# Optimization experiments

Measured on AMD Instinct MI355X. Metric: run time of the kernel, lower is better.

## Reference

```python
import jax, jax.numpy as jnp
import numpy as np

SIZE = 128      # reconstruction grid (size x size)
ANGLES = 128    # number of projection angles after interpolation
B, C, H, W = 2, 8, 128, 128  # batch, channels, detector rows (z-slices), detector cols
N_VIEWS = 8


def setup_inputs() -> dict:
    key = jax.random.key(0)
    keys = jax.random.split(key, N_VIEWS)
    return {f"f{i}": jax.random.normal(keys[i], (B, C, H, W), dtype=jnp.float32)
            for i in range(N_VIEWS)}


def _fbp(projections, size, n_angles):
    # projections: (B, C, H, V, W) -- V stacked views, W detector columns
    b, c, h, v, w = projections.shape
    # Interpolation step: resize V views -> n_angles angles (linear, half-pixel,
    # matching F.interpolate default semantics)
    sino = jax.image.resize(projections, (b, c, h, n_angles, w), method="linear")
    # Ram-Lak ramp filter along the detector-column axis
    ramp = jnp.abs(jnp.fft.fftfreq(w)).astype(jnp.float32)
    filt = jnp.real(jnp.fft.ifft(jnp.fft.fft(sino, axis=-1) * ramp, axis=-1)).astype(sino.dtype)
    # Back-projection (parallel beam, per z-slice H)
    thetas = jnp.arange(n_angles, dtype=jnp.float32) * (jnp.pi / n_angles)
    xs = jnp.arange(size, dtype=jnp.float32) - (size - 1) / 2.0
    X, Y = jnp.meshgrid(xs, xs, indexing="xy")  # (S, S)
    center = (w - 1) / 2.0

    sino_per_angle = jnp.moveaxis(filt, 3, 0)  # (A, B, C, H, W)

    def body(acc, inputs):
        theta, sino_a = inputs                       # sino_a: (B, C, H, W)
        t = X * jnp.cos(theta) + Y * jnp.sin(theta) + center  # (S, S)
        t = jnp.clip(t, 0.0, w - 1.0)
        t0 = jnp.floor(t).astype(jnp.int32)
        t1 = jnp.minimum(t0 + 1, w - 1)
        w1 = (t - t0).astype(sino_a.dtype)
        v0 = sino_a[..., t0]                         # (B, C, H, S, S) gather
        v1 = sino_a[..., t1]
        acc = acc + v0 * (1.0 - w1) + v1 * w1
        return acc, None

    acc0 = jnp.zeros((b, c, h, size, size), dtype=sino.dtype)
    vol, _ = jax.lax.scan(body, acc0, (thetas, sino_per_angle))
    return vol * (jnp.pi / (2.0 * n_angles))


def reference(f0, f1, f2, f3, f4, f5, f6, f7):
    # torch.cat([f.unsqueeze(3) for f in features], dim=3) == stack on new axis 3
    projections = jnp.stack([f0, f1, f2, f3, f4, f5, f6, f7], axis=3)  # (B,C,H,V,W)
    return _fbp(projections, SIZE, ANGLES)
```

## Files before the change

kernel.cpp:

```cpp
#include <hip/hip_runtime.h>
#include <math.h>

#define W 128
#define NANG 128
#define SZ 128
#define NV 8
#define NROWS 2048
#define K_DIM 1024
#define NPIX 16384
#define OUT_SCALE 0.012271846303085130f

typedef _Float16 f16x8 __attribute__((ext_vector_type(8)));
typedef _Float16 f16x4 __attribute__((ext_vector_type(4)));
typedef float    f32x4 __attribute__((ext_vector_type(4)));

#define PF_OFF 36864
#define WV_OFF (36864 + (size_t)NROWS * K_DIM * 2)

struct Ptrs8 { const float* p[8]; };

__device__ __forceinline__ void glds16(const void* g, void* l) {
    __builtin_amdgcn_global_load_lds(
        (const __attribute__((address_space(1))) void*)g,
        (__attribute__((address_space(3))) void*)l, 16, 0, 0);
}

#define FS_A 136
#define PREP_FG_BLOCKS 256

union PrepLds {
    struct {
        _Float16 sA[64 * FS_A];
        _Float16 sB[128 * FS_A];
        float    kl[W];
    } fg;
    struct {
        float  wrow[8 * K_DIM];
        float2 cst[NANG];
    } wv;
};

__global__ __launch_bounds__(256)
void k_prep(Ptrs8 in, _Float16* __restrict__ pf, _Float16* __restrict__ wv) {
    __shared__ PrepLds u;
    const int tid = threadIdx.x;

    if (blockIdx.x < PREP_FG_BLOCKS) {
        const int blk  = blockIdx.x;
        const int lane = tid & 63, wave = tid >> 6;
        const int fr = lane & 15, fg = lane >> 4;

        if (tid < W) {
            const int d = tid;
            const float w0 = 6.283185307179586f / (float)W * (float)d;
            float s = 0.f;
            for (int f = 1; f < 64; ++f)
                s = fmaf((float)f, __cosf(w0 * (float)f), s);
            s = 2.f * s + 64.f * ((d & 1) ? -1.f : 1.f);
            u.fg.kl[d] = s * (1.f / (float)(W * W));
        }
        {
            const int i   = tid >> 5;
            const int pos = (tid & 31) * 4;
#pragma unroll
            for (int v = 0; v < NV; ++v) {
                float4 x = *(const float4*)(in.p[v] + (size_t)(blk * 8 + i) * W + pos);
                f16x4 h = { (_Float16)x.x, (_Float16)x.y, (_Float16)x.z, (_Float16)x.w };
                *(f16x4*)&u.fg.sA[(i * 8 + v) * FS_A + pos] = h;
            }
        }
        __syncthreads();
        for (int e = tid; e < W * W; e += 256) {
            const int t = e >> 7, s = e & 127;
            u.fg.sB[t * FS_A + s] = (_Float16)u.fg.kl[(t - s) & (W - 1)];
        }
        __syncthreads();

        f32x4 acc[8] = {};
#pragma unroll
        for (int kb = 0; kb < W; kb += 32) {
            f16x8 af = *(const f16x8*)&u.fg.sA[(wave * 16 + fr) * FS_A + kb + fg * 8];
#pragma unroll
            for (int nt = 0; nt < 8; ++nt) {
                f16x8 bf = *(const f16x8*)&u.fg.sB[(nt * 16 + fr) * FS_A + kb + fg * 8];
                acc[nt] = __builtin_amdgcn_mfma_f32_16x16x32_f16(af, bf, acc[nt], 0, 0, 0);
            }
        }
#pragma unroll
        for (int nt = 0; nt < 8; ++nt) {
            int m = blk * 64 + wave * 16 + fg * 4;
            int n = nt * 16 + fr;
#pragma unroll
            for (int rr = 0; rr < 4; ++rr)
                pf[(size_t)(m + rr) * W + n] = (_Float16)acc[nt][rr];
        }
    } else {
        const int p0 = (blockIdx.x - PREP_FG_BLOCKS) * 8;
        if (tid < NANG) {
            float th = (float)tid * ((float)M_PI / (float)NANG);
            u.wv.cst[tid] = make_float2(cosf(th), sinf(th));
        }
        for (int i = tid; i < 8 * K_DIM; i += 256) u.wv.wrow[i] = 0.f;
        __syncthreads();
        const int px  = tid >> 5;
        const int sub = tid & 31;
        const int p = p0 + px;
        const float x = (float)(p & 127) - 63.5f;
        const float y = (float)(p >> 7) - 63.5f;
        float* prow = &u.wv.wrow[px * K_DIM];
        for (int a = sub; a < NANG; a += 32) {
            float2 c = u.wv.cst[a];
            float t = fmaf(x, c.x, fmaf(y, c.y, 63.5f));
            t = fminf(fmaxf(t, 0.f), 127.f);
            float tf = fminf(floorf(t), 126.f);
            int   ti = (int)tf;
            float wt = t - tf;
            float src = ((float)a + 0.5f) * 0.0625f - 0.5f;
            src = fminf(fmaxf(src, 0.f), 7.f);
            float vf = floorf(src);
            int   v0 = (int)vf;
            int   v1 = v0 + 1 < NV ? v0 + 1 : NV - 1;
            float wa = src - vf;
            float wA0 = (1.f - wa) * OUT_SCALE;
            atomicAdd(&prow[v0 * W + ti],     wA0 * (1.f - wt));
            atomicAdd(&prow[v0 * W + ti + 1], wA0 * wt);
            if (v1 != v0) {
                float wA1 = wa * OUT_SCALE;
                atomicAdd(&prow[v1 * W + ti],     wA1 * (1.f - wt));
                atomicAdd(&prow[v1 * W + ti + 1], wA1 * wt);
            }
        }
        __syncthreads();
        uint* wvu = (uint*)(wv + (size_t)p0 * K_DIM);
#pragma unroll
        for (int j = 0; j < 16; ++j) {
            int j2 = tid + 256 * j;
            float2 w2 = *(const float2*)&u.wv.wrow[j2 * 2];
            union { uint uu; struct { _Float16 lo, hi; } h; } pk;
            pk.h.lo = (_Float16)w2.x; pk.h.hi = (_Float16)w2.y;
            wvu[j2] = pk.uu;
        }
    }
}

#define NT 16

__device__ __forceinline__ void fencebar() {
    asm volatile("" ::: "memory");
    __builtin_amdgcn_s_barrier();
    asm volatile("" ::: "memory");
}

__device__ __forceinline__ void stage_half(const _Float16* __restrict__ G, int R0,
                                           int h, int kt, _Float16* L, int tid) {
#pragma unroll
    for (int r = 0; r < 2; ++r) {
        const int c   = r * 512 + tid;
        const int row = (h << 7) + (c >> 3);
        const int q   = c & 7;
        const _Float16* src = G + (size_t)(R0 + row) * K_DIM + kt * 64
                                + ((q ^ (row & 7)) << 3);
        _Float16* dst = L + (h << 13) + ((r * 512 + (tid & 448)) << 3);
        glds16(src, dst);
    }
}

__device__ __forceinline__ f16x8 frag(const _Float16* L, int row, int q) {
    return *(const f16x8*)(L + row * 64 + ((q ^ (row & 7)) << 3));
}

__global__ __launch_bounds__(512, 2)
void k_gemm(const _Float16* __restrict__ A,
            const _Float16* __restrict__ Bm,
            float* __restrict__ out) {
    __shared__ _Float16 lds[65536];
    const int tid  = threadIdx.x;
    const int lane = tid & 63, wid = tid >> 6;
    const int wm = wid >> 2, wn = wid & 3;
    const int fr = lane & 15, fg = lane >> 4;

    const int flat = blockIdx.y * 64 + blockIdx.x;
    const int x    = flat & 7;
    const int idx  = flat >> 3;
    const int m0 = (idx >> 3) * 256;
    const int n0 = (x * 8 + (idx & 7)) * 256;

    _Float16* const A0 = lds;
    _Float16* const B0 = lds + 16384;
    _Float16* const A1 = lds + 32768;
    _Float16* const B1 = lds + 49152;

    stage_half(Bm, n0, 0, 0, B0, tid);
    stage_half(A,  m0, 0, 0, A0, tid);
    stage_half(Bm, n0, 1, 0, B0, tid);
    stage_half(A,  m0, 1, 0, A0, tid);
    stage_half(Bm, n0, 0, 1, B1, tid);
    stage_half(A,  m0, 0, 1, A1, tid);
    asm volatile("s_waitcnt vmcnt(4)" ::: "memory");
    fencebar();

    f32x4 acc[8][4] = {};
    f16x8 af[4][2], bf[4][2];
    const int ar = wm * 128 + fr;
    const int br = wn * 64 + fr;

    auto tile = [&](int t, _Float16* Ab, _Float16* Bb, _Float16* An, _Float16* Bn)
        __attribute__((always_inline)) {
        if (t + 1 < NT) stage_half(Bm, n0, 1, t + 1, Bn, tid);
#pragma unroll
        for (int i = 0; i < 4; ++i) {
            af[i][0] = frag(Ab, ar + i * 16, fg);
            af[i][1] = frag(Ab, ar + i * 16, 4 + fg);
        }
#pragma unroll
        for (int j = 0; j < 2; ++j) {
            bf[j][0] = frag(Bb, br + j * 16, fg);
            bf[j][1] = frag(Bb, br + j * 16, 4 + fg);
        }
        __builtin_amdgcn_s_setprio(1);
#pragma unroll
        for (int i = 0; i < 4; ++i)
#pragma unroll
            for (int j = 0; j < 2; ++j) {
                acc[i][j] = __builtin_amdgcn_mfma_f32_16x16x32_f16(af[i][0], bf[j][0], acc[i][j], 0, 0, 0);
                acc[i][j] = __builtin_amdgcn_mfma_f32_16x16x32_f16(af[i][1], bf[j][1], acc[i][j], 0, 0, 0);
            }
        __builtin_amdgcn_s_setprio(0);
        asm volatile("s_waitcnt lgkmcnt(0)" ::: "memory");
        fencebar();
        if (t + 1 < NT) stage_half(A, m0, 1, t + 1, An, tid);
#pragma unroll
        for (int j = 2; j < 4; ++j) {
            bf[j][0] = frag(Bb, br + j * 16, fg);
            bf[j][1] = frag(Bb, br + j * 16, 4 + fg);
        }
        __builtin_amdgcn_s_setprio(1);
#pragma unroll
        for (int i = 0; i < 4; ++i)
#pragma unroll
            for (int j = 2; j < 4; ++j) {
                acc[i][j] = __builtin_amdgcn_mfma_f32_16x16x32_f16(af[i][0], bf[j][0], acc[i][j], 0, 0, 0);
                acc[i][j] = __builtin_amdgcn_mfma_f32_16x16x32_f16(af[i][1], bf[j][1], acc[i][j], 0, 0, 0);
            }
        __builtin_amdgcn_s_setprio(0);
        asm volatile("s_waitcnt lgkmcnt(0)" ::: "memory");
        fencebar();
        if (t + 2 < NT) stage_half(Bm, n0, 0, t + 2, Bb, tid);
#pragma unroll
        for (int i = 0; i < 4; ++i) {
            af[i][0] = frag(Ab, ar + 64 + i * 16, fg);
            af[i][1] = frag(Ab, ar + 64 + i * 16, 4 + fg);
        }
        __builtin_amdgcn_s_setprio(1);
#pragma unroll
        for (int i = 0; i < 4; ++i)
#pragma unroll
            for (int j = 2; j < 4; ++j) {
                acc[4 + i][j] = __builtin_amdgcn_mfma_f32_16x16x32_f16(af[i][0], bf[j][0], acc[4 + i][j], 0, 0, 0);
                acc[4 + i][j] = __builtin_amdgcn_mfma_f32_16x16x32_f16(af[i][1], bf[j][1], acc[4 + i][j], 0, 0, 0);
            }
        __builtin_amdgcn_s_setprio(0);
        asm volatile("s_waitcnt lgkmcnt(0)" ::: "memory");
        fencebar();
        if (t + 2 < NT) stage_half(A, m0, 0, t + 2, Ab, tid);
        __builtin_amdgcn_s_setprio(1);
#pragma unroll
        for (int i = 0; i < 4; ++i)
#pragma unroll
            for (int j = 0; j < 2; ++j) {
                acc[4 + i][j] = __builtin_amdgcn_mfma_f32_16x16x32_f16(af[i][0], bf[j][0], acc[4 + i][j], 0, 0, 0);
                acc[4 + i][j] = __builtin_amdgcn_mfma_f32_16x16x32_f16(af[i][1], bf[j][1], acc[4 + i][j], 0, 0, 0);
            }
        __builtin_amdgcn_s_setprio(0);
        if (t + 2 < NT)      asm volatile("s_waitcnt vmcnt(4)" ::: "memory");
        else if (t + 1 < NT) asm volatile("s_waitcnt vmcnt(0)" ::: "memory");
        fencebar();
    };

    for (int tt = 0; tt < NT; tt += 2) {
        tile(tt,     A0, B0, A1, B1);
        tile(tt + 1, A1, B1, A0, B0);
    }

#pragma unroll
    for (int i = 0; i < 8; ++i) {
#pragma unroll
        for (int j = 0; j < 4; ++j) {
            const int m = m0 + wm * 128 + i * 16 + fg * 4;
            const int n = n0 + wn * 64 + j * 16 + fr;
            float* op = out + (size_t)m * NPIX + n;
#pragma unroll
            for (int rr = 0; rr < 4; ++rr)
                op[(size_t)rr * NPIX] = acc[i][j][rr];
        }
    }
}

extern "C" void kernel_launch(void* const* d_in, const int* in_sizes, int n_in,
                              void* d_out, int out_size, void* d_ws, size_t ws_size,
                              hipStream_t stream) {
    _Float16*   pf = (_Float16*)((char*)d_ws + PF_OFF);
    _Float16*   wv = (_Float16*)((char*)d_ws + WV_OFF);

    Ptrs8 in;
    for (int i = 0; i < NV; ++i) in.p[i] = (const float*)d_in[i];

    k_prep<<<PREP_FG_BLOCKS + NPIX / 8, 256, 0, stream>>>(in, pf, wv);
    dim3 grid(NPIX / 256, NROWS / 256);
    k_gemm<<<grid, 512, 0, stream>>>(pf, wv, (float*)d_out);
}
```

Baseline: 258.0 us.

## Shrink GEMM tiles to 128x128 with BK=32 and 256-thread blocks

Replaces the 256x256 tile, 512-thread GEMM (BK=64, 128KB LDS, split-phase staging) with a 128x128 tile, 256-thread kernel using BK=32 double buffering and 32KB LDS. The aim is higher occupancy (4 blocks per CU) and more blocks to fill the machine, replacing the intricate interleaved staging schedule with a simpler full-stage-then-compute loop. In exchange, global traffic per flop doubles, and each K step waits for all outstanding loads (vmcnt(0)), which can expose memory latency.

```diff
diff --git a/kernel.cpp b/kernel.cpp
--- a/kernel.cpp
+++ b/kernel.cpp
@@ -143,7 +143,7 @@
     }
 }
 
-#define NT 16
+#define NT3 32
 
 __device__ __forceinline__ void fencebar() {
     asm volatile("" ::: "memory");
@@ -151,142 +151,89 @@
     asm volatile("" ::: "memory");
 }
 
-__device__ __forceinline__ void stage_half(const _Float16* __restrict__ G, int R0,
-                                           int h, int kt, _Float16* L, int tid) {
+__device__ __forceinline__ void stage3(const _Float16* __restrict__ G, int R0,
+                                       int kt, _Float16* L, int tid) {
 #pragma unroll
     for (int r = 0; r < 2; ++r) {
-        const int c   = r * 512 + tid;
-        const int row = (h << 7) + (c >> 3);
-        const int q   = c & 7;
-        const _Float16* src = G + (size_t)(R0 + row) * K_DIM + kt * 64
-                                + ((q ^ (row & 7)) << 3);
-        _Float16* dst = L + (h << 13) + ((r * 512 + (tid & 448)) << 3);
+        const int c   = r * 256 + tid;
+        const int row = c >> 2;
+        const int q   = c & 3;
+        const _Float16* src = G + (size_t)(R0 + row) * K_DIM + kt * 32
+                                + ((q ^ (row & 3)) << 3);
+        _Float16* dst = L + ((r * 256 + (tid & 192)) << 3);
         glds16(src, dst);
     }
 }
 
-__device__ __forceinline__ f16x8 frag(const _Float16* L, int row, int q) {
-    return *(const f16x8*)(L + row * 64 + ((q ^ (row & 7)) << 3));
-}
-
-__global__ __launch_bounds__(512, 2)
+__device__ __forceinline__ f16x8 frag3(const _Float16* L, int row, int q) {
+    return *(const f16x8*)(L + row * 32 + ((q ^ (row & 3)) << 3));
+}
+
+__global__ __launch_bounds__(256, 4)
 void k_gemm(const _Float16* __restrict__ A,
             const _Float16* __restrict__ Bm,
             float* __restrict__ out) {
-    __shared__ _Float16 lds[65536];
+    __shared__ _Float16 lds[16384];
     const int tid  = threadIdx.x;
     const int lane = tid & 63, wid = tid >> 6;
-    const int wm = wid >> 2, wn = wid & 3;
+    const int wm = wid >> 1, wn = wid & 1;
     const int fr = lane & 15, fg = lane >> 4;
 
-    const int flat = blockIdx.y * 64 + blockIdx.x;
+    const int flat = blockIdx.x;
     const int x    = flat & 7;
     const int idx  = flat >> 3;
-    const int m0 = (idx >> 3) * 256;
-    const int n0 = (x * 8 + (idx & 7)) * 256;
+    const int m0 = (idx & 15) * 128;
+    const int n0 = (x * 16 + (idx >> 4)) * 128;
 
     _Float16* const A0 = lds;
-    _Float16* const B0 = lds + 16384;
-    _Float16* const A1 = lds + 32768;
-    _Float16* const B1 = lds + 49152;
-
-    stage_half(Bm, n0, 0, 0, B0, tid);
-    stage_half(A,  m0, 0, 0, A0, tid);
-    stage_half(Bm, n0, 1, 0, B0, tid);
-    stage_half(A,  m0, 1, 0, A0, tid);
-    stage_half(Bm, n0, 0, 1, B1, tid);
-    stage_half(A,  m0, 0, 1, A1, tid);
-    asm volatile("s_waitcnt vmcnt(4)" ::: "memory");
+    _Float16* const B0 = lds + 4096;
+    _Float16* const A1 = lds + 8192;
+    _Float16* const B1 = lds + 12288;
+
+    stage3(A,  m0, 0, A0, tid);
+    stage3(Bm, n0, 0, B0, tid);
+    asm volatile("s_waitcnt vmcnt(0)" ::: "memory");
     fencebar();
 
-    f32x4 acc[8][4] = {};
-    f16x8 af[4][2], bf[4][2];
-    const int ar = wm * 128 + fr;
+    f32x4 acc[4][4] = {};
+    f16x8 af[4], bf[4];
+    const int ar = wm * 64 + fr;
     const int br = wn * 64 + fr;
 
     auto tile = [&](int t, _Float16* Ab, _Float16* Bb, _Float16* An, _Float16* Bn)
         __attribute__((always_inline)) {
-        if (t + 1 < NT) stage_half(Bm, n0, 1, t + 1, Bn, tid);
-#pragma unroll
-        for (int i = 0; i < 4; ++i) {
-            af[i][0] = frag(Ab, ar + i * 16, fg);
-            af[i][1] = frag(Ab, ar + i * 16, 4 + fg);
-        }
-#pragma unroll
-        for (int j = 0; j < 2; ++j) {
-            bf[j][0] = frag(Bb, br + j * 16, fg);
-            bf[j][1] = frag(Bb, br + j * 16, 4 + fg);
-        }
+        if (t + 1 < NT3) {
+            stage3(A,  m0, t + 1, An, tid);
+            stage3(Bm, n0, t + 1, Bn, tid);
+        }
+#pragma unroll
+        for (int i = 0; i < 4; ++i) af[i] = frag3(Ab, ar + i * 16, fg);
+#pragma unroll
+        for (int j = 0; j < 4; ++j) bf[j] = frag3(Bb, br + j * 16, fg);
         __builtin_amdgcn_s_setprio(1);
 #pragma unroll
         for (int i = 0; i < 4; ++i)
 #pragma unroll
-            for (int j = 0; j < 2; ++j) {
-                acc[i][j] = __builtin_amdgcn_mfma_f32_16x16x32_f16(af[i][0], bf[j][0], acc[i][j], 0, 0, 0);
-                acc[i][j] = __builtin_amdgcn_mfma_f32_16x16x32_f16(af[i][1], bf[j][1], acc[i][j], 0, 0, 0);
-            }
+            for (int j = 0; j < 4; ++j)
+                acc[i][j] = __builtin_amdgcn_mfma_f32_16x16x32_f16(
+                    af[i], bf[j], acc[i][j], 0, 0, 0);
         __builtin_amdgcn_s_setprio(0);
         asm volatile("s_waitcnt lgkmcnt(0)" ::: "memory");
-        fencebar();
-        if (t + 1 < NT) stage_half(A, m0, 1, t + 1, An, tid);
-#pragma unroll
-        for (int j = 2; j < 4; ++j) {
-            bf[j][0] = frag(Bb, br + j * 16, fg);
-            bf[j][1] = frag(Bb, br + j * 16, 4 + fg);
-        }
-        __builtin_amdgcn_s_setprio(1);
-#pragma unroll
-        for (int i = 0; i < 4; ++i)
-#pragma unroll
-            for (int j = 2; j < 4; ++j) {
-                acc[i][j] = __builtin_amdgcn_mfma_f32_16x16x32_f16(af[i][0], bf[j][0], acc[i][j], 0, 0, 0);
-                acc[i][j] = __builtin_amdgcn_mfma_f32_16x16x32_f16(af[i][1], bf[j][1], acc[i][j], 0, 0, 0);
-            }
-        __builtin_amdgcn_s_setprio(0);
-        asm volatile("s_waitcnt lgkmcnt(0)" ::: "memory");
-        fencebar();
-        if (t + 2 < NT) stage_half(Bm, n0, 0, t + 2, Bb, tid);
-#pragma unroll
-        for (int i = 0; i < 4; ++i) {
-            af[i][0] = frag(Ab, ar + 64 + i * 16, fg);
-            af[i][1] = frag(Ab, ar + 64 + i * 16, 4 + fg);
-        }
-        __builtin_amdgcn_s_setprio(1);
-#pragma unroll
-        for (int i = 0; i < 4; ++i)
-#pragma unroll
-            for (int j = 2; j < 4; ++j) {
-                acc[4 + i][j] = __builtin_amdgcn_mfma_f32_16x16x32_f16(af[i][0], bf[j][0], acc[4 + i][j], 0, 0, 0);
-                acc[4 + i][j] = __builtin_amdgcn_mfma_f32_16x16x32_f16(af[i][1], bf[j][1], acc[4 + i][j], 0, 0, 0);
-            }
-        __builtin_amdgcn_s_setprio(0);
-        asm volatile("s_waitcnt lgkmcnt(0)" ::: "memory");
-        fencebar();
-        if (t + 2 < NT) stage_half(A, m0, 0, t + 2, Ab, tid);
-        __builtin_amdgcn_s_setprio(1);
-#pragma unroll
-        for (int i = 0; i < 4; ++i)
-#pragma unroll
-            for (int j = 0; j < 2; ++j) {
-                acc[4 + i][j] = __builtin_amdgcn_mfma_f32_16x16x32_f16(af[i][0], bf[j][0], acc[4 + i][j], 0, 0, 0);
-                acc[4 + i][j] = __builtin_amdgcn_mfma_f32_16x16x32_f16(af[i][1], bf[j][1], acc[4 + i][j], 0, 0, 0);
-            }
-        __builtin_amdgcn_s_setprio(0);
-        if (t + 2 < NT)      asm volatile("s_waitcnt vmcnt(4)" ::: "memory");
-        else if (t + 1 < NT) asm volatile("s_waitcnt vmcnt(0)" ::: "memory");
+        if (t + 1 < NT3)
+            asm volatile("s_waitcnt vmcnt(0)" ::: "memory");
         fencebar();
     };
 
-    for (int tt = 0; tt < NT; tt += 2) {
+    for (int tt = 0; tt < NT3; tt += 2) {
         tile(tt,     A0, B0, A1, B1);
         tile(tt + 1, A1, B1, A0, B0);
     }
 
 #pragma unroll
-    for (int i = 0; i < 8; ++i) {
+    for (int i = 0; i < 4; ++i) {
 #pragma unroll
         for (int j = 0; j < 4; ++j) {
-            const int m = m0 + wm * 128 + i * 16 + fg * 4;
+            const int m = m0 + wm * 64 + i * 16 + fg * 4;
             const int n = n0 + wn * 64 + j * 16 + fr;
             float* op = out + (size_t)m * NPIX + n;
 #pragma unroll
@@ -306,6 +253,5 @@
     for (int i = 0; i < NV; ++i) in.p[i] = (const float*)d_in[i];
 
     k_prep<<<PREP_FG_BLOCKS + NPIX / 8, 256, 0, stream>>>(in, pf, wv);
-    dim3 grid(NPIX / 256, NROWS / 256);
-    k_gemm<<<grid, 512, 0, stream>>>(pf, wv, (float*)d_out);
-}
+    k_gemm<<<(NROWS / 128) * (NPIX / 128), 256, 0, stream>>>(pf, wv, (float*)d_out);
+}
```

Result: no change. 260.3 us (+0.9%).
